# Performance work log

Hardware: AMD Instinct MI355X
Metric: run time of the kernel (lower is better)

## Reference

```python
import jax, jax.numpy as jnp
from jax import lax
import numpy as np

# dims
N_DIA, DLEN = 48, 64            # 48 dialogues, 64 utterances each
N = N_DIA * DLEN                # total utterances = 3072
D = 512                         # n_dim (modal feature dim)
H = 512                         # nhidden
NL = 2                          # GCNII layers
NS = 2                          # n_speakers
ALPHA, LAMDA = 0.1, 0.5
PI = float(np.pi)
SCALE = 0.99999                 # acos clamp factor from original code


def setup_inputs() -> dict:
    key = jax.random.key(0)
    ks = jax.random.split(key, 8)
    a = jax.random.normal(ks[0], (N, D), jnp.float32)
    v = jax.random.normal(ks[1], (N, D), jnp.float32)
    l = jax.random.normal(ks[2], (N, D), jnp.float32)
    qmask = jax.random.uniform(ks[3], (DLEN, N_DIA, NS), jnp.float32)
    dia_len = np.full((N_DIA,), DLEN, dtype=np.int64)  # static segment lengths
    # learned params
    W_spk = 0.02 * jax.random.normal(ks[4], (NS, D), jnp.float32)      # speaker_embeddings
    W0 = jax.random.normal(ks[5], (D, H), jnp.float32) / np.sqrt(D)    # graph_net.fcs[0]
    b0 = jnp.zeros((H,), jnp.float32)
    Wg = jax.random.normal(ks[6], (NL, H, H), jnp.float32) / np.sqrt(H)  # GCNII conv weights
    return {"a": a, "v": v, "l": l, "qmask": qmask, "dia_len": dia_len,
            "W_spk": W_spk, "W0": W0, "b0": b0, "Wg": Wg}


def _angular_sim(cs):
    # 1 - acos(cs*0.99999)/pi, clipped for numerical safety of acos
    return 1.0 - jnp.arccos(jnp.clip(cs * SCALE, -SCALE, SCALE)) / PI


def _build_adj(feats, seg_mask):
    # feats: list of 3 arrays [N, D]; seg_mask: [N, N] same-dialogue block mask
    n = feats[0].shape[0]
    normed = [f * jax.lax.rsqrt(jnp.sum(f * f, axis=1, keepdims=True)) for f in feats]
    adj = jnp.zeros((3 * n, 3 * n), feats[0].dtype)
    ar = jnp.arange(n)
    for m in range(3):
        for nn_ in range(3):
            if m == nn_:
                # within-modality: block-diagonal (per dialogue) angular cosine similarity
                sim = _angular_sim(normed[m] @ normed[m].T) * seg_mask
                adj = adj.at[m * n:(m + 1) * n, nn_ * n:(nn_ + 1) * n].set(sim)
            else:
                # cross-modality: only diagonal (same utterance) entries
                cs = jnp.sum(normed[m] * normed[nn_], axis=1)
                adj = adj.at[m * n + ar, nn_ * n + ar].set(_angular_sim(cs))
    # symmetric degree normalization D^-1/2 A D^-1/2
    dinv = jax.lax.rsqrt(adj.sum(axis=1))
    return adj * dinv[:, None] * dinv[None, :]


def reference(a, v, l, qmask, dia_len, W_spk, W0, b0, Wg):
    dl = np.asarray(dia_len)
    nb = dl.shape[0]
    # node -> (position-in-dialogue, dialogue-id), static from dia_len
    dia_id = np.repeat(np.arange(nb), dl)
    pos = np.concatenate([np.arange(x) for x in dl])
    qflat = qmask[pos, dia_id]                 # [N, NS], matches torch.cat order
    spk_idx = jnp.argmax(qflat, axis=-1)       # [N]
    l = l + W_spk[spk_idx]                     # use_speaker=True, 'l' in modals

    seg = jnp.asarray(dia_id)
    seg_mask = (seg[:, None] == seg[None, :]).astype(a.dtype)  # [N, N]
    adj = _build_adj([a, v, l], seg_mask)      # [3N, 3N]

    x = jnp.concatenate([a, v, l], axis=0)     # [3N, D]
    # GCNII_lyc (eval mode: dropout is identity)
    h0 = jax.nn.relu(x @ W0 + b0)              # [3N, H]
    thetas = jnp.log(LAMDA / jnp.arange(1, NL + 1, dtype=x.dtype) + 1.0)

    def step(h, wt):
        W, theta = wt
        hi = adj @ h
        support = (1.0 - ALPHA) * hi + ALPHA * h0   # variant=False
        h = jax.nn.relu(theta * (support @ W) + (1.0 - theta) * support)
        return h, None

    h, _ = lax.scan(step, h0, (Wg, thetas))
    feat = jnp.concatenate([x, h], axis=-1)    # use_residue=True -> [3N, D+H]
    n = a.shape[0]
    # regroup per-utterance modal features: [N, 3*(D+H)]
    out = jnp.concatenate([feat[:n], feat[n:2 * n], feat[2 * n:3 * n]], axis=-1)
    return out
```

## Files before the change

kernel.cpp:

```cpp
#include <hip/hip_runtime.h>
#include <math.h>

#define N_DIA 48
#define NTOT  3072
#define DD    512
#define M3    9216
#define SEG   ((size_t)NTOT * DD)

#define SCALE_F 0.99999f
#define PI_F    3.14159274101257324f

typedef __attribute__((ext_vector_type(8))) short frag8;
typedef __attribute__((ext_vector_type(4))) float f32x4;

__device__ __forceinline__ float ang_sim(float cs) {
    float cc = cs * SCALE_F;
    cc = fminf(fmaxf(cc, -SCALE_F), SCALE_F);
    return 1.0f - acosf(cc) / PI_F;
}
__device__ __forceinline__ unsigned short f2bf(float x) {
    union { float f; unsigned int u; } c; c.f = x;
    unsigned int r = c.u + 0x7fffu + ((c.u >> 16) & 1u);
    return (unsigned short)(r >> 16);
}
__device__ __forceinline__ float bf2f(unsigned short h) {
    union { unsigned int u; float f; } c; c.u = ((unsigned int)h) << 16;
    return c.f;
}
__device__ __forceinline__ void gload16(const unsigned short* g, unsigned short* s) {
    __builtin_amdgcn_global_load_lds(
        (const __attribute__((address_space(1))) unsigned int*)g,
        (__attribute__((address_space(3))) unsigned int*)s, 16, 0, 0);
}

__global__ __launch_bounds__(256) void k_pre_wt(
    const float* __restrict__ a, const float* __restrict__ v,
    const float* __restrict__ l, const float* __restrict__ qmask,
    const float* __restrict__ Wspk, const float* __restrict__ W0,
    const float* __restrict__ Wg,
    float* __restrict__ out, unsigned short* __restrict__ xb,
    float* __restrict__ invn, float* __restrict__ cross,
    unsigned short* __restrict__ Wt)
{
    __shared__ float tile[32][33];
    int b = blockIdx.x;
    if (b < 768) {
        int wv = threadIdx.x >> 6, t = threadIdx.x & 63;
        int i = b * 4 + wv;
        int pos = i & 63, dia = i >> 6;
        int qb = (pos * N_DIA + dia) * 2;
        float q0 = qmask[qb], q1 = qmask[qb + 1];
        int spk = (q0 >= q1) ? 0 : 1;
        const float4* av4 = (const float4*)(a + (size_t)i * DD);
        const float4* vv4 = (const float4*)(v + (size_t)i * DD);
        const float4* lv4 = (const float4*)(l + (size_t)i * DD);
        const float4* wv4 = (const float4*)(Wspk + (size_t)spk * DD);
        float* ob = out + (size_t)i * 3072;
        float saa = 0, svv = 0, sll = 0, sav = 0, sal = 0, svl = 0;
#pragma unroll
        for (int e = 0; e < 2; e++) {
            int idx = e * 64 + t;
            float4 xa = av4[idx], xv = vv4[idx], xd = lv4[idx], xw = wv4[idx];
            float4 xL = make_float4(xd.x + xw.x, xd.y + xw.y, xd.z + xw.z, xd.w + xw.w);
            *(float4*)(ob + idx * 4)        = xa;
            *(float4*)(ob + 1024 + idx * 4) = xv;
            *(float4*)(ob + 2048 + idx * 4) = xL;
            ushort4 ya, yv, yl;
            ya.x = f2bf(xa.x); ya.y = f2bf(xa.y); ya.z = f2bf(xa.z); ya.w = f2bf(xa.w);
            yv.x = f2bf(xv.x); yv.y = f2bf(xv.y); yv.z = f2bf(xv.z); yv.w = f2bf(xv.w);
            yl.x = f2bf(xL.x); yl.y = f2bf(xL.y); yl.z = f2bf(xL.z); yl.w = f2bf(xL.w);
            *(ushort4*)(xb + (size_t)i * DD + idx * 4) = ya;
            *(ushort4*)(xb + SEG + (size_t)i * DD + idx * 4) = yv;
            *(ushort4*)(xb + 2 * SEG + (size_t)i * DD + idx * 4) = yl;
            saa += xa.x * xa.x + xa.y * xa.y + xa.z * xa.z + xa.w * xa.w;
            svv += xv.x * xv.x + xv.y * xv.y + xv.z * xv.z + xv.w * xv.w;
            sll += xL.x * xL.x + xL.y * xL.y + xL.z * xL.z + xL.w * xL.w;
            sav += xa.x * xv.x + xa.y * xv.y + xa.z * xv.z + xa.w * xv.w;
            sal += xa.x * xL.x + xa.y * xL.y + xa.z * xL.z + xa.w * xL.w;
            svl += xv.x * xL.x + xv.y * xL.y + xv.z * xL.z + xv.w * xL.w;
        }
#pragma unroll
        for (int off = 32; off; off >>= 1) {
            saa += __shfl_down(saa, off, 64);
            svv += __shfl_down(svv, off, 64);
            sll += __shfl_down(sll, off, 64);
            sav += __shfl_down(sav, off, 64);
            sal += __shfl_down(sal, off, 64);
            svl += __shfl_down(svl, off, 64);
        }
        if (t == 0) {
            float ina = 1.0f / sqrtf(saa);
            float inv_ = 1.0f / sqrtf(svv);
            float inl = 1.0f / sqrtf(sll);
            invn[i] = ina; invn[NTOT + i] = inv_; invn[2 * NTOT + i] = inl;
            cross[i]            = ang_sim(sav * ina * inv_);
            cross[NTOT + i]     = ang_sim(sal * ina * inl);
            cross[2 * NTOT + i] = ang_sim(svl * inv_ * inl);
        }
    } else {
        int idx = b - 768;
        int mm = idx >> 8;
        int by = (idx >> 4) & 15, bx = idx & 15;
        const float* W = (mm == 0) ? W0 : Wg + (size_t)(mm - 1) * DD * DD;
        int t = threadIdx.x, tx = t & 31, ty = t >> 5;
#pragma unroll
        for (int q = 0; q < 4; q++) {
            int k = by * 32 + ty + q * 8;
            tile[ty + q * 8][tx] = W[(size_t)k * DD + bx * 32 + tx];
        }
        __syncthreads();
#pragma unroll
        for (int q = 0; q < 4; q++) {
            int n = bx * 32 + ty + q * 8;
            Wt[(size_t)mm * DD * DD + (size_t)n * DD + by * 32 + tx] = f2bf(tile[tx][ty + q * 8]);
        }
    }
}

__global__ __launch_bounds__(256) void k_gram_mfma(
    const unsigned short* __restrict__ xb, const float* __restrict__ invn,
    const float* __restrict__ cross, float* __restrict__ blk,
    float* __restrict__ dinv)
{
    __shared__ __align__(16) unsigned short Xs[16 * 2048];
    int d = blockIdx.x, m = blockIdx.y;
    int t = threadIdx.x;
    int lane = t & 63, wv = t >> 6;
    int mrow = m * NTOT + d * 64;
    const unsigned short* src = xb + (size_t)mrow * DD;
    int sunit = ((t & 3) ^ ((t >> 2) & 3)) * 8;
#pragma unroll
    for (int c = 0; c < 16; c++) {
        gload16(src + (size_t)(t >> 2) * DD + c * 32 + sunit,
                &Xs[c * 2048 + wv * 512]);
    }
    __syncthreads();

    int rsel = lane & 15, quad = lane >> 4;
    int sq = (quad ^ (rsel & 3)) * 8;
    f32x4 acc[4];
#pragma unroll
    for (int j = 0; j < 4; j++) acc[j] = (f32x4){0.f, 0.f, 0.f, 0.f};
#pragma unroll
    for (int c = 0; c < 16; c++) {
        const unsigned short* base = &Xs[c * 2048];
        frag8 bf[4];
#pragma unroll
        for (int j = 0; j < 4; j++)
            bf[j] = *(const frag8*)&base[(j * 16 + rsel) * 32 + sq];
        frag8 af = *(const frag8*)&base[(wv * 16 + rsel) * 32 + sq];
#pragma unroll
        for (int j = 0; j < 4; j++)
            acc[j] = __builtin_amdgcn_mfma_f32_16x16x32_bf16(af, bf[j], acc[j], 0, 0, 0);
    }

    size_t bbase = (size_t)(m * N_DIA + d) * 4096;
    int rowl0 = wv * 16 + quad * 4;
    float ir[4], rs[4] = {0.f, 0.f, 0.f, 0.f};
#pragma unroll
    for (int r = 0; r < 4; r++) ir[r] = invn[mrow + rowl0 + r];
#pragma unroll
    for (int j = 0; j < 4; j++) {
        int coll = j * 16 + rsel;
        float ic = invn[mrow + coll];
#pragma unroll
        for (int r = 0; r < 4; r++) {
            float sim = ang_sim(acc[j][r] * ir[r] * ic);
            blk[bbase + (size_t)(rowl0 + r) * 64 + coll] = sim;
            rs[r] += sim;
        }
    }
#pragma unroll
    for (int off = 8; off; off >>= 1)
#pragma unroll
        for (int r = 0; r < 4; r++) rs[r] += __shfl_down(rs[r], off, 16);
    if (rsel == 0) {
#pragma unroll
        for (int r = 0; r < 4; r++) {
            int gi = d * 64 + rowl0 + r;
            float c1, c2;
            if (m == 0)      { c1 = cross[gi];        c2 = cross[NTOT + gi]; }
            else if (m == 1) { c1 = cross[gi];        c2 = cross[2 * NTOT + gi]; }
            else             { c1 = cross[NTOT + gi]; c2 = cross[2 * NTOT + gi]; }
            dinv[m * NTOT + gi] = 1.0f / sqrtf(rs[r] + c1 + c2);
        }
    }
}

__global__ __launch_bounds__(256) void k_gemm(
    const unsigned short* __restrict__ A, const unsigned short* __restrict__ W,
    const float* __restrict__ bias,
    unsigned short* __restrict__ oRows, unsigned short* __restrict__ oT,
    float theta, int mode,
    const unsigned short* __restrict__ A2, unsigned short* __restrict__ oRows2)
{
    __shared__ __align__(16) char smem[53248];
    unsigned short* const As0 = (unsigned short*)smem;
    unsigned short* const As1 = (unsigned short*)(smem + 8192);
    unsigned short* const Bs0 = (unsigned short*)(smem + 16384);
    unsigned short* const Bs1 = (unsigned short*)(smem + 32768);
    unsigned short* const tH  = (unsigned short*)smem;
    unsigned short* const tR  = (unsigned short*)(smem + 17408);
    unsigned short* const tT  = (unsigned short*)(smem + 34816);

    int t = threadIdx.x, lane = t & 63, wv = t >> 6;
    int bx = blockIdx.x, by = blockIdx.y;
    const unsigned short* Ap = A;
    unsigned short* oR = oRows;
    unsigned short* oTp = oT;
    if (by >= 144) { Ap = A2; oR = oRows2; oTp = nullptr; by -= 144; }
    int mbase = by * 64, nbase = bx * 128;
    int rsel = lane & 15, quad = lane >> 4;
    int r8 = lane >> 3, u8 = lane & 7;
    int su8 = (u8 ^ r8) << 3;

    const unsigned short* Ag = Ap + (size_t)(mbase + wv * 8 + r8) * DD + su8;
    const unsigned short* Bg = W  + (size_t)(nbase + wv * 8 + r8) * DD + su8;

    f32x4 acc[8];
#pragma unroll
    for (int i = 0; i < 8; i++) acc[i] = (f32x4){0.f, 0.f, 0.f, 0.f};

#define STAGE64(kt, Asb, Bsb) do { \
    gload16(Ag + (kt) * 64,                    (Asb) + (wv * 8) * 64); \
    gload16(Ag + (size_t)32 * DD + (kt) * 64,  (Asb) + (32 + wv * 8) * 64); \
    gload16(Bg + (kt) * 64,                    (Bsb) + (wv * 8) * 64); \
    gload16(Bg + (size_t)32 * DD + (kt) * 64,  (Bsb) + (32 + wv * 8) * 64); \
    gload16(Bg + (size_t)64 * DD + (kt) * 64,  (Bsb) + (64 + wv * 8) * 64); \
    gload16(Bg + (size_t)96 * DD + (kt) * 64,  (Bsb) + (96 + wv * 8) * 64); \
} while (0)

    STAGE64(0, As0, Bs0);
#pragma unroll
    for (int kt = 0; kt < 8; kt++) {
        __syncthreads();
        const unsigned short* Ac = (kt & 1) ? As1 : As0;
        const unsigned short* Bc = (kt & 1) ? Bs1 : Bs0;
        if (kt < 7) {
            unsigned short* An = (kt & 1) ? As0 : As1;
            unsigned short* Bn = (kt & 1) ? Bs0 : Bs1;
            STAGE64(kt + 1, An, Bn);
        }
#pragma unroll
        for (int ks = 0; ks < 2; ks++) {
            int su = (((ks << 2) + quad) ^ (rsel & 7)) << 3;
            frag8 af[4], bfr[2];
#pragma unroll
            for (int i = 0; i < 4; i++)
                af[i] = *(const frag8*)&Ac[(i * 16 + rsel) * 64 + su];
#pragma unroll
            for (int j = 0; j < 2; j++)
                bfr[j] = *(const frag8*)&Bc[(wv * 32 + j * 16 + rsel) * 64 + su];
#pragma unroll
            for (int i = 0; i < 4; i++)
#pragma unroll
                for (int j = 0; j < 2; j++)
                    acc[i * 2 + j] = __builtin_amdgcn_mfma_f32_16x16x32_bf16(
                        af[i], bfr[j], acc[i * 2 + j], 0, 0, 0);
        }
    }
#undef STAGE64
    __syncthreads();

    int r = t >> 2, c0 = (t & 3) * 32;
    if (mode == 1) {
        const unsigned short* srcA = Ap + (size_t)(mbase + r) * DD + nbase + c0;
#pragma unroll
        for (int u = 0; u < 4; u++)
            *(uint4*)&tH[r * 136 + c0 + u * 8] = *(const uint4*)(srcA + u * 8);
        __syncthreads();
    }
    float omt = 1.0f - theta;
#pragma unroll
    for (int i = 0; i < 4; i++)
#pragma unroll
        for (int j = 0; j < 2; j++) {
            int cl = wv * 32 + j * 16 + rsel;
            float bv = 0.f;
            if (mode == 0) bv = bias[nbase + cl];
            float vv[4];
#pragma unroll
            for (int rr = 0; rr < 4; rr++) {
                int rl = i * 16 + quad * 4 + rr;
                float x = acc[i * 2 + j][rr];
                if (mode == 0) x = fmaxf(x + bv, 0.f);
                else           x = theta * x + omt * bf2f(tH[rl * 136 + cl]);
                vv[rr] = x;
            }
#pragma unroll
            for (int rr = 0; rr < 4; rr++)
                tR[(i * 16 + quad * 4 + rr) * 136 + cl] = f2bf(vv[rr]);
            if (oTp) {
                ushort4 w4;
                w4.x = f2bf(vv[0]); w4.y = f2bf(vv[1]);
                w4.z = f2bf(vv[2]); w4.w = f2bf(vv[3]);
                *(ushort4*)&tT[cl * 72 + i * 16 + quad * 4] = w4;
            }
        }
    __syncthreads();
    {
        unsigned short* dst = oR + (size_t)(mbase + r) * DD + nbase + c0;
#pragma unroll
        for (int u = 0; u < 4; u++)
            *(uint4*)(dst + u * 8) = *(const uint4*)&tR[r * 136 + c0 + u * 8];
    }
    if (oTp) {
        int c = t >> 1, r0 = (t & 1) * 32;
        unsigned short* dst = oTp + (size_t)(nbase + c) * M3 + mbase + r0;
#pragma unroll
        for (int u = 0; u < 4; u++)
            *(uint4*)(dst + u * 8) = *(const uint4*)&tT[c * 72 + r0 + u * 8];
    }
}

__global__ __launch_bounds__(256) void k_adj(
    const float* __restrict__ blk, const float* __restrict__ cross,
    const float* __restrict__ dinv,
    const unsigned short* __restrict__ GT, const unsigned short* __restrict__ Gr,
    const unsigned short* __restrict__ P0,
    unsigned short* __restrict__ hout, float* __restrict__ outF, int final_mode)
{
    __shared__ __align__(16) unsigned short AdL[64 * 64];
    __shared__ __align__(16) unsigned short GTL[128 * 64];
    __shared__ __align__(16) unsigned short OT[64 * 136];
    __shared__ float dv[64];
    int ch = blockIdx.x, d = blockIdx.y, m = blockIdx.z;
    int t = threadIdx.x;
    int lane = t & 63, wv = t >> 6;
    int dbase = d * 64, cbase = ch * 128;
    int rsel = lane & 15, quad = lane >> 4;

    if (t < 64) dv[t] = dinv[m * NTOT + dbase + t];
    __syncthreads();

    size_t bbase = (size_t)(m * N_DIA + d) * 4096;
#pragma unroll
    for (int q = 0; q < 4; q++) {
        int e4 = t + 256 * q;
        int i = e4 >> 4, j4 = e4 & 15;
        float4 w = *(const float4*)(blk + bbase + (size_t)i * 64 + j4 * 4);
        float di = dv[i];
        ushort4 o;
        o.x = f2bf(w.x * di * dv[j4 * 4 + 0]);
        o.y = f2bf(w.y * di * dv[j4 * 4 + 1]);
        o.z = f2bf(w.z * di * dv[j4 * 4 + 2]);
        o.w = f2bf(w.w * di * dv[j4 * 4 + 3]);
        *(ushort4*)((char*)AdL + i * 128 + (((j4 >> 1) ^ (i & 7)) << 4) + ((j4 & 1) << 3)) = o;
    }
#pragma unroll
    for (int p = 0; p < 4; p++) {
        int e = t + 256 * p;
        int cl = e >> 3;
        int uo = e & 7;
        uint4 w = *(const uint4*)(GT + (size_t)(cbase + cl) * M3 + m * NTOT + dbase + uo * 8);
        *(uint4*)((char*)GTL + cl * 128 + ((uo ^ (cl & 7)) << 4)) = w;
    }
    __syncthreads();

    f32x4 acc[8];
#pragma unroll
    for (int i = 0; i < 8; i++) acc[i] = (f32x4){0.f, 0.f, 0.f, 0.f};
#pragma unroll
    for (int kk = 0; kk < 2; kk++) {
        int su = ((kk * 4 + quad) ^ (rsel & 7)) << 4;
        frag8 bfr[4];
#pragma unroll
        for (int it = 0; it < 4; it++)
            bfr[it] = *(const frag8*)((const char*)AdL + (it * 16 + rsel) * 128 + su);
#pragma unroll
        for (int jc = 0; jc < 2; jc++) {
            frag8 af = *(const frag8*)((const char*)GTL + (wv * 32 + jc * 16 + rsel) * 128 + su);
#pragma unroll
            for (int it = 0; it < 4; it++)
                acc[jc * 4 + it] = __builtin_amdgcn_mfma_f32_16x16x32_bf16(
                    af, bfr[it], acc[jc * 4 + it], 0, 0, 0);
        }
    }

    int n1, n2, p1, p2;
    if (m == 0)      { n1 = 1; n2 = 2; p1 = 0; p2 = 1; }
    else if (m == 1) { n1 = 0; n2 = 2; p1 = 0; p2 = 2; }
    else             { n1 = 0; n2 = 1; p1 = 1; p2 = 2; }
#pragma unroll
    for (int it = 0; it < 4; it++) {
        int il = it * 16 + rsel;
        int gi = dbase + il;
        float dm = dv[il];
        float cv1 = cross[p1 * NTOT + gi] * dm * dinv[n1 * NTOT + gi];
        float cv2 = cross[p2 * NTOT + gi] * dm * dinv[n2 * NTOT + gi];
        size_t r1 = (size_t)(n1 * NTOT + gi) * DD;
        size_t r2 = (size_t)(n2 * NTOT + gi) * DD;
        size_t r0 = (size_t)(m * NTOT + gi) * DD;
#pragma unroll
        for (int jc = 0; jc < 2; jc++) {
            int cl = wv * 32 + jc * 16 + quad * 4;
            int cg = cbase + cl;
            ushort4 u1 = *(const ushort4*)(Gr + r1 + cg);
            ushort4 u2 = *(const ushort4*)(Gr + r2 + cg);
            ushort4 u0 = *(const ushort4*)(P0 + r0 + cg);
            f32x4 aa = acc[jc * 4 + it];
            float o0 = fmaxf(0.9f * (aa[0] + cv1 * bf2f(u1.x) + cv2 * bf2f(u2.x)) + 0.1f * bf2f(u0.x), 0.f);
            float o1 = fmaxf(0.9f * (aa[1] + cv1 * bf2f(u1.y) + cv2 * bf2f(u2.y)) + 0.1f * bf2f(u0.y), 0.f);
            float o2 = fmaxf(0.9f * (aa[2] + cv1 * bf2f(u1.z) + cv2 * bf2f(u2.z)) + 0.1f * bf2f(u0.z), 0.f);
            float o3 = fmaxf(0.9f * (aa[3] + cv1 * bf2f(u1.w) + cv2 * bf2f(u2.w)) + 0.1f * bf2f(u0.w), 0.f);
            if (final_mode) {
                *(float4*)(outF + (size_t)gi * 3072 + m * 1024 + 512 + cg) =
                    make_float4(o0, o1, o2, o3);
            } else {
                ushort4 w;
                w.x = f2bf(o0); w.y = f2bf(o1); w.z = f2bf(o2); w.w = f2bf(o3);
                *(ushort4*)&OT[il * 136 + cl] = w;
            }
        }
    }
    if (!final_mode) {
        __syncthreads();
        int r = t >> 2, c0 = (t & 3) * 32;
        unsigned short* dst = hout + (size_t)(m * NTOT + dbase + r) * DD + cbase + c0;
#pragma unroll
        for (int u = 0; u < 4; u++)
            *(uint4*)(dst + u * 8) = *(const uint4*)&OT[r * 136 + c0 + u * 8];
    }
}

extern "C" void kernel_launch(void* const* d_in, const int* in_sizes, int n_in,
                              void* d_out, int out_size, void* d_ws, size_t ws_size,
                              hipStream_t stream) {
    (void)in_sizes; (void)n_in; (void)out_size; (void)ws_size;
    const float* a     = (const float*)d_in[0];
    const float* v     = (const float*)d_in[1];
    const float* l     = (const float*)d_in[2];
    const float* qmask = (const float*)d_in[3];
    const float* Wspk  = (const float*)d_in[5];
    const float* W0    = (const float*)d_in[6];
    const float* b0    = (const float*)d_in[7];
    const float* Wg    = (const float*)d_in[8];
    float* out = (float*)d_out;
    float* ws = (float*)d_ws;

    float* invn  = ws;
    float* blk   = invn + M3;
    float* cross = blk + (size_t)3 * N_DIA * 4096;
    float* dinvp = cross + M3;
    unsigned short* Wt  = (unsigned short*)(dinvp + M3);
    unsigned short* xb  = Wt + (size_t)3 * DD * DD;
    unsigned short* h0  = xb  + 3 * SEG;
    unsigned short* G1r = h0  + 3 * SEG;
    unsigned short* G1T = G1r + 3 * SEG;
    unsigned short* h1  = G1T + 3 * SEG;
    unsigned short* G2r = xb;
    unsigned short* G2T = G1r;
    unsigned short* P02 = G1T;

    const float th1 = 0.40546510810816438f;
    const float th2 = 0.22314355131420976f;

    k_pre_wt<<<1536, 256, 0, stream>>>(a, v, l, qmask, Wspk, W0, Wg, out, xb, invn, cross, Wt);
    k_gram_mfma<<<dim3(N_DIA, 3), 256, 0, stream>>>(xb, invn, cross, blk, dinvp);

    k_gemm<<<dim3(4, 144), 256, 0, stream>>>(xb, Wt, b0, h0, nullptr, 0.f, 0, nullptr, nullptr);
    k_gemm<<<dim3(4, 144), 256, 0, stream>>>(h0, Wt + (size_t)DD * DD, nullptr, G1r, G1T,
                                             th1, 1, nullptr, nullptr);
    k_adj<<<dim3(4, N_DIA, 3), 256, 0, stream>>>(blk, cross, dinvp, G1T, G1r, G1r,
                                                 h1, nullptr, 0);
    k_gemm<<<dim3(4, 288), 256, 0, stream>>>(h1, Wt + (size_t)2 * DD * DD, nullptr, G2r, G2T,
                                             th2, 1, h0, P02);
    k_adj<<<dim3(4, N_DIA, 3), 256, 0, stream>>>(blk, cross, dinvp, G2T, G2r, P02,
                                                 nullptr, out, 1);
}
```

Measured before the change: 195.1 us.

## Merge gram-similarity kernel and first projection GEMM into one launch

The per-dialogue gram/angular-similarity kernel and the mode-0 h0 = relu(xW0+b) GEMM are combined into a single kernel with 720 blocks. The first 144 blocks do the gram work and the remaining 576 do the GEMM tiles. The gram path now stages its data through 32KB of shared memory in two halves so it fits the shared GEMM buffer. The mode branch is removed from k_gemm. This saves one launch and lets the small 144-block gram job overlap with the GEMM instead of underfilling the GPU alone, at the cost of an extra sync in the gram path.

```diff
diff --git a/kernel.cpp b/kernel.cpp
--- a/kernel.cpp
+++ b/kernel.cpp
@@ -117,81 +117,170 @@
     }
 }
 
-__global__ __launch_bounds__(256) void k_gram_mfma(
-    const unsigned short* __restrict__ xb, const float* __restrict__ invn,
-    const float* __restrict__ cross, float* __restrict__ blk,
-    float* __restrict__ dinv)
+__global__ __launch_bounds__(256) void k_g0_gram(
+    const unsigned short* __restrict__ xb, const unsigned short* __restrict__ Wt,
+    const float* __restrict__ bias, unsigned short* __restrict__ h0,
+    const float* __restrict__ invn, const float* __restrict__ cross,
+    float* __restrict__ blk, float* __restrict__ dinv)
 {
-    __shared__ __align__(16) unsigned short Xs[16 * 2048];
-    int d = blockIdx.x, m = blockIdx.y;
-    int t = threadIdx.x;
-    int lane = t & 63, wv = t >> 6;
-    int mrow = m * NTOT + d * 64;
-    const unsigned short* src = xb + (size_t)mrow * DD;
-    int sunit = ((t & 3) ^ ((t >> 2) & 3)) * 8;
-#pragma unroll
-    for (int c = 0; c < 16; c++) {
-        gload16(src + (size_t)(t >> 2) * DD + c * 32 + sunit,
-                &Xs[c * 2048 + wv * 512]);
-    }
+    __shared__ __align__(16) char smem[53248];
+    int b = blockIdx.x;
+    int t = threadIdx.x, lane = t & 63, wv = t >> 6;
+    int rsel = lane & 15, quad = lane >> 4;
+
+    if (b < 144) {
+        unsigned short* Xs = (unsigned short*)smem;
+        int d = b % N_DIA, m = b / N_DIA;
+        int mrow = m * NTOT + d * 64;
+        const unsigned short* src = xb + (size_t)mrow * DD;
+        int sunit = ((t & 3) ^ ((t >> 2) & 3)) * 8;
+        int sq = (quad ^ (rsel & 3)) * 8;
+        f32x4 acc[4];
+#pragma unroll
+        for (int j = 0; j < 4; j++) acc[j] = (f32x4){0.f, 0.f, 0.f, 0.f};
+#pragma unroll
+        for (int p = 0; p < 2; p++) {
+            if (p) __syncthreads();
+#pragma unroll
+            for (int c = 0; c < 8; c++) {
+                gload16(src + (size_t)(t >> 2) * DD + (p * 8 + c) * 32 + sunit,
+                        &Xs[c * 2048 + wv * 512]);
+            }
+            __syncthreads();
+#pragma unroll
+            for (int c = 0; c < 8; c++) {
+                const unsigned short* base = &Xs[c * 2048];
+                frag8 bf[4];
+#pragma unroll
+                for (int j = 0; j < 4; j++)
+                    bf[j] = *(const frag8*)&base[(j * 16 + rsel) * 32 + sq];
+                frag8 af = *(const frag8*)&base[(wv * 16 + rsel) * 32 + sq];
+#pragma unroll
+                for (int j = 0; j < 4; j++)
+                    acc[j] = __builtin_amdgcn_mfma_f32_16x16x32_bf16(af, bf[j], acc[j], 0, 0, 0);
+            }
+        }
+
+        size_t bbase = (size_t)(m * N_DIA + d) * 4096;
+        int rowl0 = wv * 16 + quad * 4;
+        float ir[4], rs[4] = {0.f, 0.f, 0.f, 0.f};
+#pragma unroll
+        for (int r = 0; r < 4; r++) ir[r] = invn[mrow + rowl0 + r];
+#pragma unroll
+        for (int j = 0; j < 4; j++) {
+            int coll = j * 16 + rsel;
+            float ic = invn[mrow + coll];
+#pragma unroll
+            for (int r = 0; r < 4; r++) {
+                float sim = ang_sim(acc[j][r] * ir[r] * ic);
+                blk[bbase + (size_t)(rowl0 + r) * 64 + coll] = sim;
+                rs[r] += sim;
+            }
+        }
+#pragma unroll
+        for (int off = 8; off; off >>= 1)
+#pragma unroll
+            for (int r = 0; r < 4; r++) rs[r] += __shfl_down(rs[r], off, 16);
+        if (rsel == 0) {
+#pragma unroll
+            for (int r = 0; r < 4; r++) {
+                int gi = d * 64 + rowl0 + r;
+                float c1, c2;
+                if (m == 0)      { c1 = cross[gi];        c2 = cross[NTOT + gi]; }
+                else if (m == 1) { c1 = cross[gi];        c2 = cross[2 * NTOT + gi]; }
+                else             { c1 = cross[NTOT + gi]; c2 = cross[2 * NTOT + gi]; }
+                dinv[m * NTOT + gi] = 1.0f / sqrtf(rs[r] + c1 + c2);
+            }
+        }
+        return;
+    }
+
+    unsigned short* const As0 = (unsigned short*)smem;
+    unsigned short* const As1 = (unsigned short*)(smem + 8192);
+    unsigned short* const Bs0 = (unsigned short*)(smem + 16384);
+    unsigned short* const Bs1 = (unsigned short*)(smem + 32768);
+    unsigned short* const tR  = (unsigned short*)(smem + 17408);
+
+    int b2 = b - 144;
+    int bx = b2 & 3, by = b2 >> 2;
+    int mbase = by * 64, nbase = bx * 128;
+    int r8 = lane >> 3, u8 = lane & 7;
+    int su8 = (u8 ^ r8) << 3;
+
+    const unsigned short* Ag = xb + (size_t)(mbase + wv * 8 + r8) * DD + su8;
+    const unsigned short* Bg = Wt + (size_t)(nbase + wv * 8 + r8) * DD + su8;
+
+    f32x4 acc[8];
+#pragma unroll
+    for (int i = 0; i < 8; i++) acc[i] = (f32x4){0.f, 0.f, 0.f, 0.f};
+
+#define STAGE64(kt, Asb, Bsb) do { \
+    gload16(Ag + (kt) * 64,                    (Asb) + (wv * 8) * 64); \
+    gload16(Ag + (size_t)32 * DD + (kt) * 64,  (Asb) + (32 + wv * 8) * 64); \
+    gload16(Bg + (kt) * 64,                    (Bsb) + (wv * 8) * 64); \
+    gload16(Bg + (size_t)32 * DD + (kt) * 64,  (Bsb) + (32 + wv * 8) * 64); \
+    gload16(Bg + (size_t)64 * DD + (kt) * 64,  (Bsb) + (64 + wv * 8) * 64); \
+    gload16(Bg + (size_t)96 * DD + (kt) * 64,  (Bsb) + (96 + wv * 8) * 64); \
+} while (0)
+
+    STAGE64(0, As0, Bs0);
+#pragma unroll
+    for (int kt = 0; kt < 8; kt++) {
+        __syncthreads();
+        const unsigned short* Ac = (kt & 1) ? As1 : As0;
+        const unsigned short* Bc = (kt & 1) ? Bs1 : Bs0;
+        if (kt < 7) {
+            unsigned short* An = (kt & 1) ? As0 : As1;
+            unsigned short* Bn = (kt & 1) ? Bs0 : Bs1;
+            STAGE64(kt + 1, An, Bn);
+        }
+#pragma unroll
+        for (int ks = 0; ks < 2; ks++) {
+            int su = (((ks << 2) + quad) ^ (rsel & 7)) << 3;
+            frag8 af[4], bfr[2];
+#pragma unroll
+            for (int i = 0; i < 4; i++)
+                af[i] = *(const frag8*)&Ac[(i * 16 + rsel) * 64 + su];
+#pragma unroll
+            for (int j = 0; j < 2; j++)
+                bfr[j] = *(const frag8*)&Bc[(wv * 32 + j * 16 + rsel) * 64 + su];
+#pragma unroll
+            for (int i = 0; i < 4; i++)
+#pragma unroll
+                for (int j = 0; j < 2; j++)
+                    acc[i * 2 + j] = __builtin_amdgcn_mfma_f32_16x16x32_bf16(
+                        af[i], bfr[j], acc[i * 2 + j], 0, 0, 0);
+        }
+    }
+#undef STAGE64
     __syncthreads();
 
-    int rsel = lane & 15, quad = lane >> 4;
-    int sq = (quad ^ (rsel & 3)) * 8;
-    f32x4 acc[4];
-#pragma unroll
-    for (int j = 0; j < 4; j++) acc[j] = (f32x4){0.f, 0.f, 0.f, 0.f};
-#pragma unroll
-    for (int c = 0; c < 16; c++) {
-        const unsigned short* base = &Xs[c * 2048];
-        frag8 bf[4];
-#pragma unroll
-        for (int j = 0; j < 4; j++)
-            bf[j] = *(const frag8*)&base[(j * 16 + rsel) * 32 + sq];
-        frag8 af = *(const frag8*)&base[(wv * 16 + rsel) * 32 + sq];
-#pragma unroll
-        for (int j = 0; j < 4; j++)
-            acc[j] = __builtin_amdgcn_mfma_f32_16x16x32_bf16(af, bf[j], acc[j], 0, 0, 0);
-    }
-
-    size_t bbase = (size_t)(m * N_DIA + d) * 4096;
-    int rowl0 = wv * 16 + quad * 4;
-    float ir[4], rs[4] = {0.f, 0.f, 0.f, 0.f};
-#pragma unroll
-    for (int r = 0; r < 4; r++) ir[r] = invn[mrow + rowl0 + r];
-#pragma unroll
-    for (int j = 0; j < 4; j++) {
-        int coll = j * 16 + rsel;
-        float ic = invn[mrow + coll];
-#pragma unroll
-        for (int r = 0; r < 4; r++) {
-            float sim = ang_sim(acc[j][r] * ir[r] * ic);
-            blk[bbase + (size_t)(rowl0 + r) * 64 + coll] = sim;
-            rs[r] += sim;
-        }
-    }
-#pragma unroll
-    for (int off = 8; off; off >>= 1)
-#pragma unroll
-        for (int r = 0; r < 4; r++) rs[r] += __shfl_down(rs[r], off, 16);
-    if (rsel == 0) {
-#pragma unroll
-        for (int r = 0; r < 4; r++) {
-            int gi = d * 64 + rowl0 + r;
-            float c1, c2;
-            if (m == 0)      { c1 = cross[gi];        c2 = cross[NTOT + gi]; }
-            else if (m == 1) { c1 = cross[gi];        c2 = cross[2 * NTOT + gi]; }
-            else             { c1 = cross[NTOT + gi]; c2 = cross[2 * NTOT + gi]; }
-            dinv[m * NTOT + gi] = 1.0f / sqrtf(rs[r] + c1 + c2);
-        }
+#pragma unroll
+    for (int i = 0; i < 4; i++)
+#pragma unroll
+        for (int j = 0; j < 2; j++) {
+            int cl = wv * 32 + j * 16 + rsel;
+            float bv = bias[nbase + cl];
+#pragma unroll
+            for (int rr = 0; rr < 4; rr++) {
+                float x = fmaxf(acc[i * 2 + j][rr] + bv, 0.f);
+                tR[(i * 16 + quad * 4 + rr) * 136 + cl] = f2bf(x);
+            }
+        }
+    __syncthreads();
+    {
+        int r = t >> 2, c0 = (t & 3) * 32;
+        unsigned short* dst = h0 + (size_t)(mbase + r) * DD + nbase + c0;
+#pragma unroll
+        for (int u = 0; u < 4; u++)
+            *(uint4*)(dst + u * 8) = *(const uint4*)&tR[r * 136 + c0 + u * 8];
     }
 }
 
 __global__ __launch_bounds__(256) void k_gemm(
     const unsigned short* __restrict__ A, const unsigned short* __restrict__ W,
-    const float* __restrict__ bias,
     unsigned short* __restrict__ oRows, unsigned short* __restrict__ oT,
-    float theta, int mode,
+    float theta,
     const unsigned short* __restrict__ A2, unsigned short* __restrict__ oRows2)
 {
     __shared__ __align__(16) char smem[53248];
@@ -263,7 +352,7 @@
     __syncthreads();
 
     int r = t >> 2, c0 = (t & 3) * 32;
-    if (mode == 1) {
+    {
         const unsigned short* srcA = Ap + (size_t)(mbase + r) * DD + nbase + c0;
 #pragma unroll
         for (int u = 0; u < 4; u++)
@@ -276,16 +365,11 @@
 #pragma unroll
         for (int j = 0; j < 2; j++) {
             int cl = wv * 32 + j * 16 + rsel;
-            float bv = 0.f;
-            if (mode == 0) bv = bias[nbase + cl];
             float vv[4];
 #pragma unroll
             for (int rr = 0; rr < 4; rr++) {
                 int rl = i * 16 + quad * 4 + rr;
-                float x = acc[i * 2 + j][rr];
-                if (mode == 0) x = fmaxf(x + bv, 0.f);
-                else           x = theta * x + omt * bf2f(tH[rl * 136 + cl]);
-                vv[rr] = x;
+                vv[rr] = theta * acc[i * 2 + j][rr] + omt * bf2f(tH[rl * 136 + cl]);
             }
 #pragma unroll
             for (int rr = 0; rr < 4; rr++)
@@ -456,15 +540,13 @@
     const float th2 = 0.22314355131420976f;
 
     k_pre_wt<<<1536, 256, 0, stream>>>(a, v, l, qmask, Wspk, W0, Wg, out, xb, invn, cross, Wt);
-    k_gram_mfma<<<dim3(N_DIA, 3), 256, 0, stream>>>(xb, invn, cross, blk, dinvp);
-
-    k_gemm<<<dim3(4, 144), 256, 0, stream>>>(xb, Wt, b0, h0, nullptr, 0.f, 0, nullptr, nullptr);
-    k_gemm<<<dim3(4, 144), 256, 0, stream>>>(h0, Wt + (size_t)DD * DD, nullptr, G1r, G1T,
-                                             th1, 1, nullptr, nullptr);
+    k_g0_gram<<<720, 256, 0, stream>>>(xb, Wt, b0, h0, invn, cross, blk, dinvp);
+    k_gemm<<<dim3(4, 144), 256, 0, stream>>>(h0, Wt + (size_t)DD * DD, G1r, G1T,
+                                             th1, nullptr, nullptr);
     k_adj<<<dim3(4, N_DIA, 3), 256, 0, stream>>>(blk, cross, dinvp, G1T, G1r, G1r,
                                                  h1, nullptr, 0);
-    k_gemm<<<dim3(4, 288), 256, 0, stream>>>(h1, Wt + (size_t)2 * DD * DD, nullptr, G2r, G2T,
-                                             th2, 1, h0, P02);
+    k_gemm<<<dim3(4, 288), 256, 0, stream>>>(h1, Wt + (size_t)2 * DD * DD, G2r, G2T,
+                                             th2, h0, P02);
     k_adj<<<dim3(4, N_DIA, 3), 256, 0, stream>>>(blk, cross, dinvp, G2T, G2r, P02,
                                                  nullptr, out, 1);
 }
```

Measured after the change: 185.5 us. -4.9%, faster.
